# Performance work log

Measured on AMD Instinct MI355X. Metric: run time of the kernel, lower is better.

Reference implementation:

```python
import jax, jax.numpy as jnp
import numpy as np

D_MODEL = 2048
NUM_HEADS = 16
D_FF = 8192
BATCH = 4
SEQ = 2048


def setup_inputs() -> dict:
    key = jax.random.key(0)
    ks = jax.random.split(key, 16)
    s_attn = 1.0 / np.sqrt(D_MODEL)
    s_ff1 = 1.0 / np.sqrt(D_MODEL)
    s_ff2 = 1.0 / np.sqrt(D_FF)
    return {
        "x": jax.random.normal(ks[0], (BATCH, SEQ, D_MODEL), dtype=jnp.float32),
        "Wq": jax.random.normal(ks[1], (D_MODEL, D_MODEL), dtype=jnp.float32) * s_attn,
        "bq": jnp.zeros((D_MODEL,), dtype=jnp.float32),
        "Wk": jax.random.normal(ks[2], (D_MODEL, D_MODEL), dtype=jnp.float32) * s_attn,
        "bk": jnp.zeros((D_MODEL,), dtype=jnp.float32),
        "Wv": jax.random.normal(ks[3], (D_MODEL, D_MODEL), dtype=jnp.float32) * s_attn,
        "bv": jnp.zeros((D_MODEL,), dtype=jnp.float32),
        "Wo": jax.random.normal(ks[4], (D_MODEL, D_MODEL), dtype=jnp.float32) * s_attn,
        "bo": jnp.zeros((D_MODEL,), dtype=jnp.float32),
        "W1": jax.random.normal(ks[5], (D_MODEL, D_FF), dtype=jnp.float32) * s_ff1,
        "b1": jnp.zeros((D_FF,), dtype=jnp.float32),
        "W2": jax.random.normal(ks[6], (D_FF, D_MODEL), dtype=jnp.float32) * s_ff2,
        "b2": jnp.zeros((D_MODEL,), dtype=jnp.float32),
        "ln1_g": jnp.ones((D_MODEL,), dtype=jnp.float32),
        "ln1_b": jnp.zeros((D_MODEL,), dtype=jnp.float32),
        "ln2_g": jnp.ones((D_MODEL,), dtype=jnp.float32),
        "ln2_b": jnp.zeros((D_MODEL,), dtype=jnp.float32),
    }


def _layer_norm(x, g, b, eps=1e-5):
    mu = jnp.mean(x, axis=-1, keepdims=True)
    var = jnp.mean(jnp.square(x - mu), axis=-1, keepdims=True)
    return (x - mu) * jax.lax.rsqrt(var + eps) * g + b


def _attention(h, Wq, bq, Wk, bk, Wv, bv, Wo, bo):
    B, S, D = h.shape
    H = NUM_HEADS
    dk = D // H
    q = (h @ Wq + bq).reshape(B, S, H, dk).transpose(0, 2, 1, 3)  # bhsd
    k = (h @ Wk + bk).reshape(B, S, H, dk).transpose(0, 2, 1, 3)
    v = (h @ Wv + bv).reshape(B, S, H, dk).transpose(0, 2, 1, 3)
    logits = jnp.einsum("bhqd,bhkd->bhqk", q, k) / jnp.sqrt(jnp.float32(dk))
    causal = jnp.triu(jnp.ones((S, S), dtype=bool), k=1)  # True above diagonal
    logits = jnp.where(causal, -jnp.inf, logits)
    attn = jax.nn.softmax(logits, axis=-1)
    out = jnp.einsum("bhqk,bhkd->bhqd", attn, v)
    out = out.transpose(0, 2, 1, 3).reshape(B, S, D)
    return out @ Wo + bo


def reference(x, Wq, bq, Wk, bk, Wv, bv, Wo, bo, W1, b1, W2, b2,
              ln1_g, ln1_b, ln2_g, ln2_b):
    # Pre-LN attention block + residual
    h = _layer_norm(x, ln1_g, ln1_b)
    x = x + _attention(h, Wq, bq, Wk, bk, Wv, bv, Wo, bo)
    # Pre-LN FFN block + residual (GELU activation)
    h = _layer_norm(x, ln2_g, ln2_b)
    ff = jax.nn.gelu(h @ W1 + b1, approximate=False) @ W2 + b2
    return x + ff
```

## Files before the change

kernel.cpp:

```cpp
#include <hip/hip_runtime.h>
#include <hip/hip_bf16.h>

#define D_MODEL 2048
#define NUM_HEADS 16
#define D_FF 8192
#define BATCH 4
#define SEQ 2048
#define DK 128
#define MTOT (BATCH * SEQ)

typedef __attribute__((ext_vector_type(8))) short short8;
typedef __attribute__((ext_vector_type(4))) short short4v;
typedef __attribute__((ext_vector_type(4))) float f32x4;

#define MFMA16(a, b, c) __builtin_amdgcn_mfma_f32_16x16x32_bf16(a, b, c, 0, 0, 0)

#define GLOAD16(gp, lp)                                                        \
  __builtin_amdgcn_global_load_lds(                                            \
      (const __attribute__((address_space(1))) void*)(gp),                     \
      (__attribute__((address_space(3))) void*)(lp), 16, 0, 0)

static __device__ __forceinline__ unsigned short f2bf(float f) {
  return __builtin_bit_cast(unsigned short, __float2bfloat16(f));
}

__global__ __launch_bounds__(256) void transpose_cvt_kernel(
    const float* __restrict__ in, __hip_bfloat16* __restrict__ out, int K, int N) {
  __shared__ float tile[32][33];
  const int n0 = blockIdx.x * 32, k0 = blockIdx.y * 32;
  const int tx = threadIdx.x & 31, ty = threadIdx.x >> 5;
#pragma unroll
  for (int i = 0; i < 4; ++i)
    tile[ty + i * 8][tx] = in[(size_t)(k0 + ty + i * 8) * N + n0 + tx];
  __syncthreads();
#pragma unroll
  for (int i = 0; i < 4; ++i)
    out[(size_t)(n0 + ty + i * 8) * K + k0 + tx] = __float2bfloat16(tile[tx][ty + i * 8]);
}

__global__ __launch_bounds__(256) void layernorm_kernel(
    const float* __restrict__ x, const float* __restrict__ g,
    const float* __restrict__ bta, __hip_bfloat16* __restrict__ out) {
  const int row = blockIdx.x;
  const int tid = threadIdx.x;
  const float* xr = x + (size_t)row * D_MODEL;
  float4 v0 = *(const float4*)(xr + tid * 8);
  float4 v1 = *(const float4*)(xr + tid * 8 + 4);
  float s = v0.x + v0.y + v0.z + v0.w + v1.x + v1.y + v1.z + v1.w;
  float q = v0.x * v0.x + v0.y * v0.y + v0.z * v0.z + v0.w * v0.w +
            v1.x * v1.x + v1.y * v1.y + v1.z * v1.z + v1.w * v1.w;
#pragma unroll
  for (int off = 1; off < 64; off <<= 1) {
    s += __shfl_xor(s, off);
    q += __shfl_xor(q, off);
  }
  __shared__ float rs[4], rq[4];
  if ((tid & 63) == 0) {
    rs[tid >> 6] = s;
    rq[tid >> 6] = q;
  }
  __syncthreads();
  s = rs[0] + rs[1] + rs[2] + rs[3];
  q = rq[0] + rq[1] + rq[2] + rq[3];
  const float mu = s * (1.0f / D_MODEL);
  const float var = q * (1.0f / D_MODEL) - mu * mu;
  const float rstd = rsqrtf(var + 1e-5f);
  float4 g0 = *(const float4*)(g + tid * 8);
  float4 g1 = *(const float4*)(g + tid * 8 + 4);
  float4 b0 = *(const float4*)(bta + tid * 8);
  float4 b1 = *(const float4*)(bta + tid * 8 + 4);
  short8 o;
  o[0] = (short)f2bf((v0.x - mu) * rstd * g0.x + b0.x);
  o[1] = (short)f2bf((v0.y - mu) * rstd * g0.y + b0.y);
  o[2] = (short)f2bf((v0.z - mu) * rstd * g0.z + b0.z);
  o[3] = (short)f2bf((v0.w - mu) * rstd * g0.w + b0.w);
  o[4] = (short)f2bf((v1.x - mu) * rstd * g1.x + b1.x);
  o[5] = (short)f2bf((v1.y - mu) * rstd * g1.y + b1.y);
  o[6] = (short)f2bf((v1.z - mu) * rstd * g1.z + b1.z);
  o[7] = (short)f2bf((v1.w - mu) * rstd * g1.w + b1.w);
  *(short8*)(out + (size_t)row * D_MODEL + tid * 8) = o;
}

enum { EPI_BF16 = 0, EPI_VT = 1, EPI_RESID = 2, EPI_GELU = 3 };

#define AF_MFMA_PHASE(FI0)                                                     \
  {                                                                            \
    const int raA = wm + (FI0) * 16 + l15;                                     \
    const int raB = wm + ((FI0) + 1) * 16 + l15;                               \
    short8 aA0 = *(const short8*)(db + raA * 128 + ((lg ^ (raA & 7)) << 4));   \
    short8 aB0 = *(const short8*)(db + raB * 128 + ((lg ^ (raB & 7)) << 4));   \
    short8 aA1 =                                                               \
        *(const short8*)(db + raA * 128 + (((4 + lg) ^ (raA & 7)) << 4));      \
    short8 aB1 =                                                               \
        *(const short8*)(db + raB * 128 + (((4 + lg) ^ (raB & 7)) << 4));      \
    __builtin_amdgcn_s_barrier();                                              \
    asm volatile("s_waitcnt lgkmcnt(0)" ::: "memory");                         \
    __builtin_amdgcn_sched_barrier(0);                                         \
    __builtin_amdgcn_s_setprio(1);                                             \
    _Pragma("unroll") for (int fj = 0; fj < 4; ++fj)                           \
        acc[FI0][fj] = MFMA16(aA0, bf0[fj], acc[FI0][fj]);                     \
    _Pragma("unroll") for (int fj = 0; fj < 4; ++fj)                           \
        acc[(FI0) + 1][fj] = MFMA16(aB0, bf0[fj], acc[(FI0) + 1][fj]);         \
    _Pragma("unroll") for (int fj = 0; fj < 4; ++fj)                           \
        acc[FI0][fj] = MFMA16(aA1, bf1[fj], acc[FI0][fj]);                     \
    _Pragma("unroll") for (int fj = 0; fj < 4; ++fj)                           \
        acc[(FI0) + 1][fj] = MFMA16(aB1, bf1[fj], acc[(FI0) + 1][fj]);         \
    __builtin_amdgcn_s_setprio(0);                                             \
  }

template <int EPI>
__global__ __launch_bounds__(512, 2) void gemm_kernel(
    const __hip_bfloat16* __restrict__ A, const __hip_bfloat16* __restrict__ Bt,
    const float* __restrict__ bias, const float* __restrict__ resid,
    void* __restrict__ outv, int M, int N, int K) {
  __shared__ __align__(16) unsigned char lds[2][65536];
  const int tid = threadIdx.x;
  const int lane = tid & 63, w = tid >> 6;
  const int l15 = lane & 15, lg = lane >> 4;
  const int d = blockIdx.x;
  const int x = d & 7;
  const int i = d >> 3;
  const int cC = (i & 7) + 8 * (i >> 5);
  const int rC = x + 8 * ((i >> 3) & 3);
  const int m0 = rC * 256, n0 = cC * 256;
  const int wm = (w >> 2) * 128, wn = (w & 3) * 64;

  f32x4 acc[8][4] = {};

  const int row8 = lane >> 3;
  const int g8 = (lane & 7) ^ row8;
  const int wa = (w & 3) + ((w >> 2) * 16);

  auto stA = [&](int tt, int c) {
    GLOAD16(A + (size_t)(m0 + c * 8 + row8) * K + (size_t)tt * 64 + g8 * 8,
            lds[tt & 1] + c * 1024);
  };
  auto stB = [&](int tt, int c) {
    GLOAD16(Bt + (size_t)(n0 + c * 8 + row8) * K + (size_t)tt * 64 + g8 * 8,
            lds[tt & 1] + 32768 + c * 1024);
  };

  const int nt = K >> 6;

  stB(0, w); stB(0, 8 + w); stA(0, wa);
  stB(0, 16 + w); stB(0, 24 + w); stA(0, wa + 4);
  stA(0, wa + 8); stA(0, wa + 12);
  stB(1, w); stB(1, 8 + w); stA(1, wa);
  stB(1, 16 + w); stB(1, 24 + w); stA(1, wa + 4);
  stA(1, wa + 8);
  asm volatile("s_waitcnt vmcnt(7)" ::: "memory");
  __builtin_amdgcn_s_barrier();

  for (int t = 0; t < nt; ++t) {
    const unsigned char* db = lds[t & 1];
    const bool s1 = (t + 1 < nt), s2 = (t + 2 < nt);
    short8 bf0[4], bf1[4];
    if (s1) stA(t + 1, wa + 12);
#pragma unroll
    for (int f = 0; f < 4; ++f) {
      const int rb = wn + f * 16 + l15;
      bf0[f] = *(const short8*)(db + 32768 + rb * 128 + ((lg ^ (rb & 7)) << 4));
      bf1[f] =
          *(const short8*)(db + 32768 + rb * 128 + (((4 + lg) ^ (rb & 7)) << 4));
    }
    AF_MFMA_PHASE(0)
    __builtin_amdgcn_s_barrier();
    if (s2) { stB(t + 2, w); stB(t + 2, 8 + w); stA(t + 2, wa); }
    AF_MFMA_PHASE(2)
    __builtin_amdgcn_s_barrier();
    if (s2) { stB(t + 2, 16 + w); stB(t + 2, 24 + w); stA(t + 2, wa + 4); }
    AF_MFMA_PHASE(4)
    __builtin_amdgcn_s_barrier();
    if (s2) stA(t + 2, wa + 8);
    AF_MFMA_PHASE(6)
    if (s2)
      asm volatile("s_waitcnt vmcnt(7)" ::: "memory");
    else
      asm volatile("s_waitcnt vmcnt(0)" ::: "memory");
    __builtin_amdgcn_s_barrier();
  }

#pragma unroll
  for (int fi = 0; fi < 8; ++fi) {
#pragma unroll
    for (int fj = 0; fj < 4; ++fj) {
      const int mb = m0 + wm + fi * 16 + lg * 4;
      const int n = n0 + wn + fj * 16 + l15;
      const float bv = bias ? bias[n] : 0.0f;
      if constexpr (EPI == EPI_VT) {
        const int bb = mb >> 11, ss = mb & (SEQ - 1);
        const int hh = n >> 7, dd = n & (DK - 1);
        short4v pk;
#pragma unroll
        for (int r = 0; r < 4; ++r) pk[r] = (short)f2bf(acc[fi][fj][r] + bv);
        __hip_bfloat16* o = (__hip_bfloat16*)outv;
        *(short4v*)(o + ((size_t)((bb * NUM_HEADS + hh) * DK + dd)) * SEQ + ss) = pk;
      } else {
#pragma unroll
        for (int r = 0; r < 4; ++r) {
          const int m = mb + r;
          const float v = acc[fi][fj][r] + bv;
          if constexpr (EPI == EPI_BF16) {
            ((__hip_bfloat16*)outv)[(size_t)m * N + n] = __float2bfloat16(v);
          } else if constexpr (EPI == EPI_GELU) {
            const float ge = 0.5f * v * (1.0f + erff(v * 0.70710678118654752f));
            ((__hip_bfloat16*)outv)[(size_t)m * N + n] = __float2bfloat16(ge);
          } else {
            ((float*)outv)[(size_t)m * N + n] = resid[(size_t)m * N + n] + v;
          }
        }
      }
    }
  }
}

__global__ __launch_bounds__(512, 4) void attn_kernel(
    const __hip_bfloat16* __restrict__ Qm, const __hip_bfloat16* __restrict__ Km,
    const __hip_bfloat16* __restrict__ Vt, __hip_bfloat16* __restrict__ Om) {
  __shared__ __align__(16) unsigned char Kl[2][16384];
  __shared__ __align__(16) unsigned char Vl[2][16384];
  const int tid = threadIdx.x;
  const int lane = tid & 63, w = tid >> 6;
  const int l15 = lane & 15, lg = lane >> 4;
  const int bh = blockIdx.y, b = bh >> 4, h = bh & 15;
  const int q0 = ((int)gridDim.x - 1 - (int)blockIdx.x) * 128;
  const int qw = q0 + w * 16;
  const int row8 = lane >> 3;
  const int nt = (q0 >> 6) + 2;

  short8 qf[4];
  const __hip_bfloat16* qbase = Qm + (size_t)(b * SEQ + qw + l15) * D_MODEL + h * DK;
#pragma unroll
  for (int ks = 0; ks < 4; ++ks) qf[ks] = *(const short8*)(qbase + ks * 32 + lg * 8);

  float m_run = -1e30f, l_run = 0.0f;
  f32x4 acc_o[8];
#pragma unroll
  for (int fd = 0; fd < 8; ++fd) acc_o[fd] = (f32x4){0.f, 0.f, 0.f, 0.f};

  auto STAGE = [&](int tt) {
    unsigned char* kb = Kl[tt & 1];
    unsigned char* vb = Vl[tt & 1];
    const int t0s = tt * 64;
#pragma unroll
    for (int i = 0; i < 2; ++i) {
      const int c = w * 2 + i;
      const int row = c * 4 + lg;
      const int gcb = l15 ^ (row & 7);
      GLOAD16(Km + (size_t)(b * SEQ + t0s + row) * D_MODEL + h * DK + gcb * 8,
              kb + c * 1024);
    }
#pragma unroll
    for (int i = 0; i < 2; ++i) {
      const int c = w * 2 + i;
      const int row = c * 8 + row8;
      const int gcb = (lane & 7) ^ (row & 7);
      GLOAD16(Vt + (size_t)(bh * DK + row) * SEQ + t0s + gcb * 8, vb + c * 1024);
    }
  };

  STAGE(0);
  for (int t = 0; t < nt; ++t) {
    const int t0 = t * 64;
    if (t + 1 < nt) {
      STAGE(t + 1);
      asm volatile("s_waitcnt vmcnt(4)" ::: "memory");
    } else {
      asm volatile("s_waitcnt vmcnt(0)" ::: "memory");
    }
    __builtin_amdgcn_s_barrier();
    asm volatile("" ::: "memory");
    if (t0 <= qw + 15) {
      const unsigned char* kb = Kl[t & 1];
      const unsigned char* vb = Vl[t & 1];
      f32x4 sacc[4];
#pragma unroll
      for (int fn = 0; fn < 4; ++fn) sacc[fn] = (f32x4){0.f, 0.f, 0.f, 0.f};
      __builtin_amdgcn_s_setprio(1);
#pragma unroll
      for (int ks = 0; ks < 4; ++ks) {
        const int cb = ks * 4 + lg;
#pragma unroll
        for (int fn = 0; fn < 4; ++fn) {
          const int rn = fn * 16 + l15;
          short8 kf = *(const short8*)(kb + rn * 256 + ((cb ^ (rn & 7)) << 4));
          sacc[fn] = MFMA16(kf, qf[ks], sacc[fn]);
        }
      }
      __builtin_amdgcn_s_setprio(0);
      const float scale = 0.088388347648318447f;
      const int qg = qw + l15;
      float mt = -1e30f;
#pragma unroll
      for (int fn = 0; fn < 4; ++fn) {
        const int keyb = t0 + fn * 16 + lg * 4;
#pragma unroll
        for (int r = 0; r < 4; ++r) {
          float sv = sacc[fn][r] * scale;
          sv = (keyb + r <= qg) ? sv : -1e30f;
          sacc[fn][r] = sv;
          mt = fmaxf(mt, sv);
        }
      }
      mt = fmaxf(mt, __shfl_xor(mt, 16));
      mt = fmaxf(mt, __shfl_xor(mt, 32));
      const bool defer = __all(mt <= m_run + 8.0f);
      float alpha = 1.0f;
      if (!defer) {
        const float mnew = fmaxf(m_run, mt);
        alpha = __expf(m_run - mnew);
        m_run = mnew;
      }
      float ls = 0.0f;
#pragma unroll
      for (int fn = 0; fn < 4; ++fn)
#pragma unroll
        for (int r = 0; r < 4; ++r) {
          const float p = __expf(sacc[fn][r] - m_run);
          sacc[fn][r] = p;
          ls += p;
        }
      ls += __shfl_xor(ls, 16);
      ls += __shfl_xor(ls, 32);
      l_run = (defer ? l_run : l_run * alpha) + ls;
      if (!defer) {
        float abr[4];
#pragma unroll
        for (int r = 0; r < 4; ++r) abr[r] = __shfl(alpha, lg * 4 + r);
#pragma unroll
        for (int fd = 0; fd < 8; ++fd)
#pragma unroll
          for (int r = 0; r < 4; ++r) acc_o[fd][r] *= abr[r];
      }
      const int srcLo = l15 + 16 * (2 * (lg & 1));
      const int srcHi = srcLo + 16;
      const int hi = lg >> 1;
#pragma unroll
      for (int s = 0; s < 2; ++s) {
        short8 pf;
#pragma unroll
        for (int j = 0; j < 4; ++j) {
          const float v0 = __shfl(sacc[2 * s][j], srcLo);
          const float v1 = __shfl(sacc[2 * s + 1][j], srcLo);
          pf[j] = (short)f2bf(hi ? v1 : v0);
          const float w0 = __shfl(sacc[2 * s][j], srcHi);
          const float w1 = __shfl(sacc[2 * s + 1][j], srcHi);
          pf[4 + j] = (short)f2bf(hi ? w1 : w0);
        }
        const int cb = s * 4 + lg;
        __builtin_amdgcn_s_setprio(1);
#pragma unroll
        for (int fd = 0; fd < 8; ++fd) {
          const int rv = fd * 16 + l15;
          short8 vf = *(const short8*)(vb + rv * 128 + ((cb ^ (rv & 7)) << 4));
          acc_o[fd] = MFMA16(pf, vf, acc_o[fd]);
        }
        __builtin_amdgcn_s_setprio(0);
      }
    }
    asm volatile("" ::: "memory");
    __builtin_amdgcn_s_barrier();
    asm volatile("" ::: "memory");
  }
  float linv[4];
#pragma unroll
  for (int r = 0; r < 4; ++r) linv[r] = __shfl(l_run, lg * 4 + r);
#pragma unroll
  for (int r = 0; r < 4; ++r) {
    const float inv = 1.0f / linv[r];
    const int qg = qw + lg * 4 + r;
    __hip_bfloat16* ob = Om + (size_t)(b * SEQ + qg) * D_MODEL + h * DK + l15;
#pragma unroll
    for (int fd = 0; fd < 8; ++fd)
      ob[fd * 16] = __float2bfloat16(acc_o[fd][r] * inv);
  }
}

extern "C" void kernel_launch(void* const* d_in, const int* in_sizes, int n_in,
                              void* d_out, int out_size, void* d_ws, size_t ws_size,
                              hipStream_t stream) {
  (void)in_sizes; (void)n_in; (void)out_size;
  const size_t MB = 1024 * 1024;
  if (ws_size < 192 * MB) return;

  const float* x  = (const float*)d_in[0];
  const float* Wq = (const float*)d_in[1];
  const float* bq = (const float*)d_in[2];
  const float* Wk = (const float*)d_in[3];
  const float* bk = (const float*)d_in[4];
  const float* Wv = (const float*)d_in[5];
  const float* bv = (const float*)d_in[6];
  const float* Wo = (const float*)d_in[7];
  const float* bo = (const float*)d_in[8];
  const float* W1 = (const float*)d_in[9];
  const float* b1 = (const float*)d_in[10];
  const float* W2 = (const float*)d_in[11];
  const float* b2 = (const float*)d_in[12];
  const float* g1 = (const float*)d_in[13];
  const float* be1 = (const float*)d_in[14];
  const float* g2 = (const float*)d_in[15];
  const float* be2 = (const float*)d_in[16];

  char* ws = (char*)d_ws;
  __hip_bfloat16* Hb  = (__hip_bfloat16*)(ws + 0 * MB);
  __hip_bfloat16* Qb  = (__hip_bfloat16*)(ws + 32 * MB);
  __hip_bfloat16* Kb  = (__hip_bfloat16*)(ws + 64 * MB);
  __hip_bfloat16* Vtb = (__hip_bfloat16*)(ws + 96 * MB);
  __hip_bfloat16* AOb = (__hip_bfloat16*)(ws + 128 * MB);
  __hip_bfloat16* FF1 = (__hip_bfloat16*)(ws + 32 * MB);
  __hip_bfloat16* WqT = (__hip_bfloat16*)(ws + 160 * MB);
  __hip_bfloat16* WkT = (__hip_bfloat16*)(ws + 168 * MB);
  __hip_bfloat16* WvT = (__hip_bfloat16*)(ws + 176 * MB);
  __hip_bfloat16* WoT = (__hip_bfloat16*)(ws + 184 * MB);
  __hip_bfloat16* W1T = (__hip_bfloat16*)(ws + 160 * MB);
  __hip_bfloat16* W2T = (__hip_bfloat16*)(ws + 160 * MB);
  float* X2 = (float*)d_out;

  const dim3 tb(256);
  transpose_cvt_kernel<<<dim3(64, 64), tb, 0, stream>>>(Wq, WqT, 2048, 2048);
  transpose_cvt_kernel<<<dim3(64, 64), tb, 0, stream>>>(Wk, WkT, 2048, 2048);
  transpose_cvt_kernel<<<dim3(64, 64), tb, 0, stream>>>(Wv, WvT, 2048, 2048);
  transpose_cvt_kernel<<<dim3(64, 64), tb, 0, stream>>>(Wo, WoT, 2048, 2048);

  layernorm_kernel<<<MTOT, tb, 0, stream>>>(x, g1, be1, Hb);

  gemm_kernel<EPI_BF16><<<256, 512, 0, stream>>>(Hb, WqT, bq, nullptr, Qb, MTOT, 2048, 2048);
  gemm_kernel<EPI_BF16><<<256, 512, 0, stream>>>(Hb, WkT, bk, nullptr, Kb, MTOT, 2048, 2048);
  gemm_kernel<EPI_VT><<<256, 512, 0, stream>>>(Hb, WvT, bv, nullptr, Vtb, MTOT, 2048, 2048);

  attn_kernel<<<dim3(SEQ / 128, BATCH * NUM_HEADS), dim3(512), 0, stream>>>(Qb, Kb, Vtb, AOb);

  gemm_kernel<EPI_RESID><<<256, 512, 0, stream>>>(AOb, WoT, bo, x, X2, MTOT, 2048, 2048);

  layernorm_kernel<<<MTOT, tb, 0, stream>>>(X2, g2, be2, Hb);

  transpose_cvt_kernel<<<dim3(256, 64), tb, 0, stream>>>(W1, W1T, 2048, 8192);
  gemm_kernel<EPI_GELU><<<1024, 512, 0, stream>>>(Hb, W1T, b1, nullptr, FF1, MTOT, 8192, 2048);
  transpose_cvt_kernel<<<dim3(64, 256), tb, 0, stream>>>(W2, W2T, 8192, 2048);
  gemm_kernel<EPI_RESID><<<256, 512, 0, stream>>>(FF1, W2T, b2, X2, X2, MTOT, 2048, 8192);
}
```

Measured before the change: 1.190 ms.

## Fuse Q/K/V projections into one GEMM and batch weight transposes

Stacks the transposed Wq/Wk/Wv weights contiguously and runs a single N=6144 GEMM with a sectioned epilogue that writes Q, K and transposed V. The four 2048x2048 weight transpose-converts become one launch over a z-dimension. Barriers are switched to inline-asm s_barrier, and the attention loop now waits on lgkmcnt before its barrier. This cuts launch count, gives a larger grid (768 blocks) for better CU fill, and reads the activation once per tile set. The QKV epilogue adds per-element branching and scalar bf16 stores.

```diff
diff --git a/kernel.cpp b/kernel.cpp
--- a/kernel.cpp
+++ b/kernel.cpp
@@ -20,6 +20,8 @@
       (const __attribute__((address_space(1))) void*)(gp),                     \
       (__attribute__((address_space(3))) void*)(lp), 16, 0, 0)
 
+#define SBAR() asm volatile("s_barrier" ::: "memory")
+
 static __device__ __forceinline__ unsigned short f2bf(float f) {
   return __builtin_bit_cast(unsigned short, __float2bfloat16(f));
 }
@@ -36,6 +38,27 @@
 #pragma unroll
   for (int i = 0; i < 4; ++i)
     out[(size_t)(n0 + ty + i * 8) * K + k0 + tx] = __float2bfloat16(tile[tx][ty + i * 8]);
+}
+
+__global__ __launch_bounds__(256) void transpose_cvt4_kernel(
+    const float* __restrict__ s0, const float* __restrict__ s1,
+    const float* __restrict__ s2, const float* __restrict__ s3,
+    __hip_bfloat16* __restrict__ d0, __hip_bfloat16* __restrict__ d1,
+    __hip_bfloat16* __restrict__ d2, __hip_bfloat16* __restrict__ d3) {
+  const int z = blockIdx.z;
+  const float* in = z == 0 ? s0 : (z == 1 ? s1 : (z == 2 ? s2 : s3));
+  __hip_bfloat16* out = z == 0 ? d0 : (z == 1 ? d1 : (z == 2 ? d2 : d3));
+  __shared__ float tile[32][33];
+  const int n0 = blockIdx.x * 32, k0 = blockIdx.y * 32;
+  const int tx = threadIdx.x & 31, ty = threadIdx.x >> 5;
+#pragma unroll
+  for (int i = 0; i < 4; ++i)
+    tile[ty + i * 8][tx] = in[(size_t)(k0 + ty + i * 8) * 2048 + n0 + tx];
+  __syncthreads();
+#pragma unroll
+  for (int i = 0; i < 4; ++i)
+    out[(size_t)(n0 + ty + i * 8) * 2048 + k0 + tx] =
+        __float2bfloat16(tile[tx][ty + i * 8]);
 }
 
 __global__ __launch_bounds__(256) void layernorm_kernel(
@@ -81,7 +104,7 @@
   *(short8*)(out + (size_t)row * D_MODEL + tid * 8) = o;
 }
 
-enum { EPI_BF16 = 0, EPI_VT = 1, EPI_RESID = 2, EPI_GELU = 3 };
+enum { EPI_BF16 = 0, EPI_VT = 1, EPI_RESID = 2, EPI_GELU = 3, EPI_QKV = 4 };
 
 #define AF_MFMA_PHASE(FI0)                                                     \
   {                                                                            \
@@ -93,7 +116,7 @@
         *(const short8*)(db + raA * 128 + (((4 + lg) ^ (raA & 7)) << 4));      \
     short8 aB1 =                                                               \
         *(const short8*)(db + raB * 128 + (((4 + lg) ^ (raB & 7)) << 4));      \
-    __builtin_amdgcn_s_barrier();                                              \
+    SBAR();                                                                    \
     asm volatile("s_waitcnt lgkmcnt(0)" ::: "memory");                         \
     __builtin_amdgcn_sched_barrier(0);                                         \
     __builtin_amdgcn_s_setprio(1);                                             \
@@ -111,8 +134,10 @@
 template <int EPI>
 __global__ __launch_bounds__(512, 2) void gemm_kernel(
     const __hip_bfloat16* __restrict__ A, const __hip_bfloat16* __restrict__ Bt,
-    const float* __restrict__ bias, const float* __restrict__ resid,
-    void* __restrict__ outv, int M, int N, int K) {
+    const float* __restrict__ bias, const float* __restrict__ bias2,
+    const float* __restrict__ bias3, const float* __restrict__ resid,
+    void* __restrict__ outv, void* __restrict__ out2, void* __restrict__ out3,
+    int M, int N, int K) {
   __shared__ __align__(16) unsigned char lds[2][65536];
   const int tid = threadIdx.x;
   const int lane = tid & 63, w = tid >> 6;
@@ -149,7 +174,7 @@
   stB(1, 16 + w); stB(1, 24 + w); stA(1, wa + 4);
   stA(1, wa + 8);
   asm volatile("s_waitcnt vmcnt(7)" ::: "memory");
-  __builtin_amdgcn_s_barrier();
+  SBAR();
 
   for (int t = 0; t < nt; ++t) {
     const unsigned char* db = lds[t & 1];
@@ -164,20 +189,20 @@
           *(const short8*)(db + 32768 + rb * 128 + (((4 + lg) ^ (rb & 7)) << 4));
     }
     AF_MFMA_PHASE(0)
-    __builtin_amdgcn_s_barrier();
+    SBAR();
     if (s2) { stB(t + 2, w); stB(t + 2, 8 + w); stA(t + 2, wa); }
     AF_MFMA_PHASE(2)
-    __builtin_amdgcn_s_barrier();
+    SBAR();
     if (s2) { stB(t + 2, 16 + w); stB(t + 2, 24 + w); stA(t + 2, wa + 4); }
     AF_MFMA_PHASE(4)
-    __builtin_amdgcn_s_barrier();
+    SBAR();
     if (s2) stA(t + 2, wa + 8);
     AF_MFMA_PHASE(6)
     if (s2)
       asm volatile("s_waitcnt vmcnt(7)" ::: "memory");
     else
       asm volatile("s_waitcnt vmcnt(0)" ::: "memory");
-    __builtin_amdgcn_s_barrier();
+    SBAR();
   }
 
 #pragma unroll
@@ -186,27 +211,47 @@
     for (int fj = 0; fj < 4; ++fj) {
       const int mb = m0 + wm + fi * 16 + lg * 4;
       const int n = n0 + wn + fj * 16 + l15;
-      const float bv = bias ? bias[n] : 0.0f;
-      if constexpr (EPI == EPI_VT) {
-        const int bb = mb >> 11, ss = mb & (SEQ - 1);
-        const int hh = n >> 7, dd = n & (DK - 1);
-        short4v pk;
-#pragma unroll
-        for (int r = 0; r < 4; ++r) pk[r] = (short)f2bf(acc[fi][fj][r] + bv);
-        __hip_bfloat16* o = (__hip_bfloat16*)outv;
-        *(short4v*)(o + ((size_t)((bb * NUM_HEADS + hh) * DK + dd)) * SEQ + ss) = pk;
+      if constexpr (EPI == EPI_QKV) {
+        const int sec = n >> 11;
+        const int nn = n & 2047;
+        const float bv = sec == 0 ? bias[nn] : (sec == 1 ? bias2[nn] : bias3[nn]);
+        if (sec < 2) {
+          __hip_bfloat16* o = sec == 0 ? (__hip_bfloat16*)outv : (__hip_bfloat16*)out2;
+#pragma unroll
+          for (int r = 0; r < 4; ++r)
+            o[(size_t)(mb + r) * 2048 + nn] = __float2bfloat16(acc[fi][fj][r] + bv);
+        } else {
+          const int bb = mb >> 11, ss = mb & (SEQ - 1);
+          const int hh = nn >> 7, dd = nn & (DK - 1);
+          short4v pk;
+#pragma unroll
+          for (int r = 0; r < 4; ++r) pk[r] = (short)f2bf(acc[fi][fj][r] + bv);
+          __hip_bfloat16* o = (__hip_bfloat16*)out3;
+          *(short4v*)(o + ((size_t)((bb * NUM_HEADS + hh) * DK + dd)) * SEQ + ss) = pk;
+        }
       } else {
-#pragma unroll
-        for (int r = 0; r < 4; ++r) {
-          const int m = mb + r;
-          const float v = acc[fi][fj][r] + bv;
-          if constexpr (EPI == EPI_BF16) {
-            ((__hip_bfloat16*)outv)[(size_t)m * N + n] = __float2bfloat16(v);
-          } else if constexpr (EPI == EPI_GELU) {
-            const float ge = 0.5f * v * (1.0f + erff(v * 0.70710678118654752f));
-            ((__hip_bfloat16*)outv)[(size_t)m * N + n] = __float2bfloat16(ge);
-          } else {
-            ((float*)outv)[(size_t)m * N + n] = resid[(size_t)m * N + n] + v;
+        const float bv = bias ? bias[n] : 0.0f;
+        if constexpr (EPI == EPI_VT) {
+          const int bb = mb >> 11, ss = mb & (SEQ - 1);
+          const int hh = n >> 7, dd = n & (DK - 1);
+          short4v pk;
+#pragma unroll
+          for (int r = 0; r < 4; ++r) pk[r] = (short)f2bf(acc[fi][fj][r] + bv);
+          __hip_bfloat16* o = (__hip_bfloat16*)outv;
+          *(short4v*)(o + ((size_t)((bb * NUM_HEADS + hh) * DK + dd)) * SEQ + ss) = pk;
+        } else {
+#pragma unroll
+          for (int r = 0; r < 4; ++r) {
+            const int m = mb + r;
+            const float v = acc[fi][fj][r] + bv;
+            if constexpr (EPI == EPI_BF16) {
+              ((__hip_bfloat16*)outv)[(size_t)m * N + n] = __float2bfloat16(v);
+            } else if constexpr (EPI == EPI_GELU) {
+              const float ge = 0.5f * v * (1.0f + erff(v * 0.70710678118654752f));
+              ((__hip_bfloat16*)outv)[(size_t)m * N + n] = __float2bfloat16(ge);
+            } else {
+              ((float*)outv)[(size_t)m * N + n] = resid[(size_t)m * N + n] + v;
+            }
           }
         }
       }
@@ -268,8 +313,7 @@
     } else {
       asm volatile("s_waitcnt vmcnt(0)" ::: "memory");
     }
-    __builtin_amdgcn_s_barrier();
-    asm volatile("" ::: "memory");
+    SBAR();
     if (t0 <= qw + 15) {
       const unsigned char* kb = Kl[t & 1];
       const unsigned char* vb = Vl[t & 1];
@@ -358,9 +402,8 @@
         __builtin_amdgcn_s_setprio(0);
       }
     }
-    asm volatile("" ::: "memory");
-    __builtin_amdgcn_s_barrier();
-    asm volatile("" ::: "memory");
+    asm volatile("s_waitcnt lgkmcnt(0)" ::: "memory");
+    SBAR();
   }
   float linv[4];
 #pragma unroll
@@ -408,6 +451,7 @@
   __hip_bfloat16* Vtb = (__hip_bfloat16*)(ws + 96 * MB);
   __hip_bfloat16* AOb = (__hip_bfloat16*)(ws + 128 * MB);
   __hip_bfloat16* FF1 = (__hip_bfloat16*)(ws + 32 * MB);
+  __hip_bfloat16* WqkvT = (__hip_bfloat16*)(ws + 160 * MB);
   __hip_bfloat16* WqT = (__hip_bfloat16*)(ws + 160 * MB);
   __hip_bfloat16* WkT = (__hip_bfloat16*)(ws + 168 * MB);
   __hip_bfloat16* WvT = (__hip_bfloat16*)(ws + 176 * MB);
@@ -417,25 +461,25 @@
   float* X2 = (float*)d_out;
 
   const dim3 tb(256);
-  transpose_cvt_kernel<<<dim3(64, 64), tb, 0, stream>>>(Wq, WqT, 2048, 2048);
-  transpose_cvt_kernel<<<dim3(64, 64), tb, 0, stream>>>(Wk, WkT, 2048, 2048);
-  transpose_cvt_kernel<<<dim3(64, 64), tb, 0, stream>>>(Wv, WvT, 2048, 2048);
-  transpose_cvt_kernel<<<dim3(64, 64), tb, 0, stream>>>(Wo, WoT, 2048, 2048);
+  transpose_cvt4_kernel<<<dim3(64, 64, 4), tb, 0, stream>>>(
+      Wq, Wk, Wv, Wo, WqT, WkT, WvT, WoT);
 
   layernorm_kernel<<<MTOT, tb, 0, stream>>>(x, g1, be1, Hb);
 
-  gemm_kernel<EPI_BF16><<<256, 512, 0, stream>>>(Hb, WqT, bq, nullptr, Qb, MTOT, 2048, 2048);
-  gemm_kernel<EPI_BF16><<<256, 512, 0, stream>>>(Hb, WkT, bk, nullptr, Kb, MTOT, 2048, 2048);
-  gemm_kernel<EPI_VT><<<256, 512, 0, stream>>>(Hb, WvT, bv, nullptr, Vtb, MTOT, 2048, 2048);
+  gemm_kernel<EPI_QKV><<<768, 512, 0, stream>>>(
+      Hb, WqkvT, bq, bk, bv, nullptr, Qb, Kb, Vtb, MTOT, 6144, 2048);
 
   attn_kernel<<<dim3(SEQ / 128, BATCH * NUM_HEADS), dim3(512), 0, stream>>>(Qb, Kb, Vtb, AOb);
 
-  gemm_kernel<EPI_RESID><<<256, 512, 0, stream>>>(AOb, WoT, bo, x, X2, MTOT, 2048, 2048);
+  gemm_kernel<EPI_RESID><<<256, 512, 0, stream>>>(
+      AOb, WoT, bo, nullptr, nullptr, x, X2, nullptr, nullptr, MTOT, 2048, 2048);
 
   layernorm_kernel<<<MTOT, tb, 0, stream>>>(X2, g2, be2, Hb);
 
   transpose_cvt_kernel<<<dim3(256, 64), tb, 0, stream>>>(W1, W1T, 2048, 8192);
-  gemm_kernel<EPI_GELU><<<1024, 512, 0, stream>>>(Hb, W1T, b1, nullptr, FF1, MTOT, 8192, 2048);
+  gemm_kernel<EPI_GELU><<<1024, 512, 0, stream>>>(
+      Hb, W1T, b1, nullptr, nullptr, nullptr, FF1, nullptr, nullptr, MTOT, 8192, 2048);
   transpose_cvt_kernel<<<dim3(64, 256), tb, 0, stream>>>(W2, W2T, 8192, 2048);
-  gemm_kernel<EPI_RESID><<<256, 512, 0, stream>>>(FF1, W2T, b2, X2, X2, MTOT, 2048, 8192);
-}
+  gemm_kernel<EPI_RESID><<<256, 512, 0, stream>>>(
+      FF1, W2T, b2, nullptr, nullptr, X2, X2, nullptr, nullptr, MTOT, 2048, 8192);
+}
```

After: 1.178 ms, median of 3. No clear change (-1.0%).
